# Optimization experiments

Measured on AMD Instinct MI355X. Metric: run time of the kernel, lower is better.

The kernel has to match this reference:

```python
import jax, jax.numpy as jnp
import numpy as np

LN_EPS = 1e-5
ROPE_BASE = 10000.0

def _rope2d_tables(height, width, dim):
    # dim = head_dim; split evenly between x (width) and y (height) axes
    dim_x = dim // 2
    dim_y = dim - dim_x
    inv_fx = 1.0 / (ROPE_BASE ** (jnp.arange(0, dim_x, 2, dtype=jnp.float32) / dim_x))
    inv_fy = 1.0 / (ROPE_BASE ** (jnp.arange(0, dim_y, 2, dtype=jnp.float32) / dim_y))
    fx = jnp.arange(width, dtype=jnp.float32)[:, None] * inv_fx[None, :]   # [W, dim_x/2]
    fy = jnp.arange(height, dtype=jnp.float32)[:, None] * inv_fy[None, :]  # [H, dim_y/2]
    cos_x = jnp.concatenate([jnp.cos(fx), jnp.cos(fx)], -1)  # [W, dim_x]
    sin_x = jnp.concatenate([jnp.sin(fx), jnp.sin(fx)], -1)
    cos_y = jnp.concatenate([jnp.cos(fy), jnp.cos(fy)], -1)  # [H, dim_y]
    sin_y = jnp.concatenate([jnp.sin(fy), jnp.sin(fy)], -1)
    cos2d = jnp.concatenate([jnp.broadcast_to(cos_x[None, :, :], (height, width, dim_x)),
                             jnp.broadcast_to(cos_y[:, None, :], (height, width, dim_y))], -1)
    sin2d = jnp.concatenate([jnp.broadcast_to(sin_x[None, :, :], (height, width, dim_x)),
                             jnp.broadcast_to(sin_y[:, None, :], (height, width, dim_y))], -1)
    return cos2d.reshape(height * width, dim), sin2d.reshape(height * width, dim)

def _apply_rope(x, cos, sin):
    # x: [..., S, D]; cos/sin broadcastable [S, D]
    d = x.shape[-1]
    x1, x2 = x[..., : d // 2], x[..., d // 2 :]
    rotated = jnp.concatenate([-x2, x1], -1)
    return x * cos + rotated * sin

def setup_inputs() -> dict:
    key = jax.random.key(0)
    ks = jax.random.split(key, 3)
    h = 1024
    x = jax.random.normal(ks[0], (1, 8192, h), dtype=jnp.float32)
    w_qkv = jax.random.normal(ks[1], (3 * h, h), dtype=jnp.float32) * (h ** -0.5)
    w_out = jax.random.normal(ks[2], (h, h), dtype=jnp.float32) * (h ** -0.5)
    return {
        "x": x, "w_qkv": w_qkv, "w_out": w_out,
        "ln_gamma": jnp.ones((h,), jnp.float32),
        "ln_beta": jnp.zeros((h,), jnp.float32),
        "height": 32, "width": 32, "frames": 8,
    }

def reference(x, w_qkv, w_out, ln_gamma, ln_beta, height, width, frames):
    B, S, hdim = x.shape
    num_heads = 16
    head_dim = hdim // num_heads
    spatial = height * width
    scale = head_dim ** -0.5

    # LayerNorm
    mu = jnp.mean(x, -1, keepdims=True)
    var = jnp.mean(jnp.square(x - mu), -1, keepdims=True)
    xn = (x - mu) * jax.lax.rsqrt(var + LN_EPS) * ln_gamma + ln_beta

    xn = xn.reshape(B * frames, spatial, hdim)
    qkv = (xn @ w_qkv.T).reshape(B * frames, spatial, 3, num_heads, head_dim)
    q, k, v = qkv[:, :, 0], qkv[:, :, 1], qkv[:, :, 2]  # [BF, S, H, D]
    q = jnp.transpose(q, (0, 2, 1, 3))  # [BF, H, S, D]
    k = jnp.transpose(k, (0, 2, 1, 3))
    v = jnp.transpose(v, (0, 2, 1, 3))

    cos, sin = _rope2d_tables(height, width, head_dim)  # [S, D]
    q = _apply_rope(q, cos, sin)
    k = _apply_rope(k, cos, sin)

    attn = jnp.einsum("bhqd,bhkd->bhqk", q, k) * scale
    attn = jax.nn.softmax(attn.astype(jnp.float32), axis=-1).astype(x.dtype)
    out = jnp.einsum("bhqk,bhkd->bhqd", attn, v)
    out = jnp.transpose(out, (0, 2, 1, 3)).reshape(B * frames, spatial, hdim)
    out = out @ w_out.T
    return out.reshape(B, S, hdim)
```

## Files before the change

### kernel.cpp

```cpp
#include <hip/hip_runtime.h>
#include <hip/hip_bf16.h>
#include <math.h>
#include <stdint.h>

typedef __bf16 bf16_t;
typedef bf16_t bf16x8 __attribute__((ext_vector_type(8)));
typedef bf16_t bf16x4 __attribute__((ext_vector_type(4)));
typedef float f32x4 __attribute__((ext_vector_type(4)));

#define GLOBAL_AS __attribute__((address_space(1)))
#define LDS_AS __attribute__((address_space(3)))

__device__ __forceinline__ void gload_lds16(const void* g, void* l) {
    __builtin_amdgcn_global_load_lds((const GLOBAL_AS unsigned int*)g,
                                     (LDS_AS unsigned int*)l, 16, 0, 0);
}

__device__ __forceinline__ f32x4 mfma16(bf16x8 a, bf16x8 b, f32x4 c) {
    return __builtin_amdgcn_mfma_f32_16x16x32_bf16(a, b, c, 0, 0, 0);
}

__global__ void prologue_kernel(const float* __restrict__ w_qkv, const float* __restrict__ w_out,
                                const float* __restrict__ x, const float* __restrict__ g,
                                const float* __restrict__ b,
                                bf16_t* __restrict__ wqb, bf16_t* __restrict__ wob,
                                bf16_t* __restrict__ xn,
                                float* __restrict__ cb, float* __restrict__ sb)
{
    __shared__ float red[8];
    const int bid = blockIdx.x;
    const int tid = threadIdx.x;

    if (bid < 3072) {
        const int i = bid * 256 + tid;
        const float4 v = ((const float4*)w_qkv)[i];
        bf16x4 o;
        o[0] = (bf16_t)v.x; o[1] = (bf16_t)v.y; o[2] = (bf16_t)v.z; o[3] = (bf16_t)v.w;
        *(bf16x4*)&wqb[(size_t)i * 4] = o;
    } else if (bid < 4096) {
        const int i = (bid - 3072) * 256 + tid;
        const float4 v = ((const float4*)w_out)[i];
        bf16x4 o;
        o[0] = (bf16_t)v.x; o[1] = (bf16_t)v.y; o[2] = (bf16_t)v.z; o[3] = (bf16_t)v.w;
        *(bf16x4*)&wob[(size_t)i * 4] = o;
    } else if (bid < 4352) {
        const int p = ((bid - 4096) << 2) | (tid >> 6);
        const int d = tid & 63;
        const int hh = p >> 5, ww = p & 31;
        const int idx = d & 15;
        const float invf = powf(10000.0f, -(float)idx / 16.0f);
        const float posv = (d >= 32) ? (float)hh : (float)ww;
        const float f = posv * invf;
        cb[p * 64 + d] = cosf(f);
        sb[p * 64 + d] = sinf(f);
    } else {
        const int row = bid - 4352;
        const float4 v = ((const float4*)(x + (size_t)row * 1024))[tid];
        float s  = v.x + v.y + v.z + v.w;
        float s2 = v.x * v.x + v.y * v.y + v.z * v.z + v.w * v.w;
        #pragma unroll
        for (int m = 1; m < 64; m <<= 1) {
            s  += __shfl_xor(s, m);
            s2 += __shfl_xor(s2, m);
        }
        const int wid = tid >> 6, lane = tid & 63;
        if (lane == 0) { red[wid] = s; red[4 + wid] = s2; }
        __syncthreads();
        s  = red[0] + red[1] + red[2] + red[3];
        s2 = red[4] + red[5] + red[6] + red[7];
        const float mu  = s * (1.0f / 1024.0f);
        const float var = s2 * (1.0f / 1024.0f) - mu * mu;
        const float rs  = rsqrtf(var + 1e-5f);
        const float4 gv = ((const float4*)g)[tid];
        const float4 bv = ((const float4*)b)[tid];
        bf16x4 o;
        o[0] = (bf16_t)((v.x - mu) * rs * gv.x + bv.x);
        o[1] = (bf16_t)((v.y - mu) * rs * gv.y + bv.y);
        o[2] = (bf16_t)((v.z - mu) * rs * gv.z + bv.z);
        o[3] = (bf16_t)((v.w - mu) * rs * gv.w + bv.w);
        *(bf16x4*)&xn[(size_t)row * 1024 + tid * 4] = o;
    }
}

template <int EPI>
__global__ __launch_bounds__(256, 2)
void gemm_bt(const bf16_t* __restrict__ A, const bf16_t* __restrict__ Bw,
             int M, int N,
             bf16_t* __restrict__ Qb, bf16_t* __restrict__ Kb, bf16_t* __restrict__ Vt,
             const float* __restrict__ cb, const float* __restrict__ sb,
             float* __restrict__ Cout)
{
    constexpr int K = 1024;
    __shared__ bf16_t Asm[2][128 * 64];
    __shared__ bf16_t Bsm[2][128 * 64];
    const int tid  = threadIdx.x;
    const int lane = tid & 63;
    const int wid  = tid >> 6;
    const int wr = wid >> 1, wc = wid & 1;
    const int lr = lane & 15;
    const int lg = lane >> 4;

    int lin = blockIdx.y * gridDim.x + blockIdx.x;
    const int cpx = (gridDim.x * gridDim.y) >> 3;
    lin = (lin & 7) * cpx + (lin >> 3);
    const int bx = lin % gridDim.x;
    const int by = lin / gridDim.x;
    const int bm = by * 128;
    const int bn = bx * 128;

    f32x4 acc[4][4] = {};

    const int r0 = tid >> 3;
    const int c8 = tid & 7;
    const int cx = c8 ^ (r0 & 7);

#define GSTAGE(b, k0) do { \
        _Pragma("unroll") \
        for (int i = 0; i < 4; ++i) { \
            gload_lds16(A  + (size_t)(bm + r0 + i * 32) * K + (k0) + cx * 8, (char*)&Asm[b][0] + i * 4096 + tid * 16); \
            gload_lds16(Bw + (size_t)(bn + r0 + i * 32) * K + (k0) + cx * 8, (char*)&Bsm[b][0] + i * 4096 + tid * 16); \
        } \
    } while (0)

    constexpr int nkt = K >> 6;
    GSTAGE(0, 0);
    GSTAGE(1, 64);

    #pragma unroll 2
    for (int t = 0; t < nkt; ++t) {
        const int cur = t & 1;
        if (t + 1 < nkt) asm volatile("s_waitcnt vmcnt(8)" ::: "memory");
        else             asm volatile("s_waitcnt vmcnt(0)" ::: "memory");
        __builtin_amdgcn_sched_barrier(0);
        __builtin_amdgcn_s_barrier();
        __builtin_amdgcn_sched_barrier(0);

        const bf16_t* As = &Asm[cur][0];
        const bf16_t* Bs = &Bsm[cur][0];
        bf16x8 af[2][4], bv[2][4];
        #pragma unroll
        for (int kk = 0; kk < 2; ++kk) {
            const int jx = ((kk * 4 + lg) ^ (lr & 7)) * 8;
            #pragma unroll
            for (int mi = 0; mi < 4; ++mi)
                af[kk][mi] = *(const bf16x8*)&As[(wr * 64 + mi * 16 + lr) * 64 + jx];
            #pragma unroll
            for (int nj = 0; nj < 4; ++nj)
                bv[kk][nj] = *(const bf16x8*)&Bs[(wc * 64 + nj * 16 + lr) * 64 + jx];
        }
        asm volatile("s_waitcnt lgkmcnt(0)" ::: "memory");
        __builtin_amdgcn_sched_barrier(0);
        __builtin_amdgcn_s_barrier();
        __builtin_amdgcn_sched_barrier(0);

        if (t + 2 < nkt) GSTAGE(cur, (t + 2) * 64);

        #pragma unroll
        for (int kk = 0; kk < 2; ++kk)
            #pragma unroll
            for (int mi = 0; mi < 4; ++mi)
                #pragma unroll
                for (int nj = 0; nj < 4; ++nj)
                    acc[mi][nj] = mfma16(af[kk][mi], bv[kk][nj], acc[mi][nj]);
    }
#undef GSTAGE

    if (EPI == 0) {
        const int sel = bn >> 10;
        if (sel < 2) {
            bf16_t* dst = sel ? Kb : Qb;
            const float qs = sel ? 1.0f : 0.18033688011112042f;
            #pragma unroll
            for (int mi = 0; mi < 4; ++mi) {
                #pragma unroll
                for (int nj = 0; nj < 2; ++nj) {
                    #pragma unroll
                    for (int r = 0; r < 4; ++r) {
                        const int m = bm + wr * 64 + mi * 16 + lg * 4 + r;
                        const int n_lo = bn + wc * 64 + nj * 16 + lr;
                        const int head = (n_lo >> 6) & 15;
                        const int d_lo = nj * 16 + lr;
                        const int pos  = m & 1023;
                        const int bfi  = m >> 10;
                        const float v_lo = acc[mi][nj][r];
                        const float v_hi = acc[mi][nj + 2][r];
                        const float c_lo = cb[pos * 64 + d_lo],      s_lo = sb[pos * 64 + d_lo];
                        const float c_hi = cb[pos * 64 + d_lo + 32], s_hi = sb[pos * 64 + d_lo + 32];
                        const size_t idx = (((size_t)(bfi * 16 + head)) << 16) + (size_t)pos * 64 + d_lo;
                        dst[idx]      = (bf16_t)((v_lo * c_lo - v_hi * s_lo) * qs);
                        dst[idx + 32] = (bf16_t)((v_hi * c_hi + v_lo * s_hi) * qs);
                    }
                }
            }
        } else {
            #pragma unroll
            for (int mi = 0; mi < 4; ++mi) {
                #pragma unroll
                for (int nj = 0; nj < 4; ++nj) {
                    bf16x4 pk;
                    #pragma unroll
                    for (int r = 0; r < 4; ++r) pk[r] = (bf16_t)acc[mi][nj][r];
                    const int m0 = bm + wr * 64 + mi * 16 + lg * 4;
                    const int n  = bn + wc * 64 + nj * 16 + lr;
                    const int head = (n >> 6) & 15;
                    const int d    = n & 63;
                    const int pos0 = m0 & 1023;
                    const int bfi  = m0 >> 10;
                    const int a = (pos0 >> 4) & 3, bb = (pos0 >> 2) & 3;
                    const int pos2 = (pos0 & ~63) | (32 * (a >> 1) + 8 * bb + 4 * (a & 1));
                    *(bf16x4*)&Vt[(((size_t)(bfi * 16 + head)) << 16) + (size_t)d * 1024 + pos2] = pk;
                }
            }
        }
    } else {
        #pragma unroll
        for (int mi = 0; mi < 4; ++mi)
            #pragma unroll
            for (int nj = 0; nj < 4; ++nj)
                #pragma unroll
                for (int r = 0; r < 4; ++r) {
                    const int m = bm + wr * 64 + mi * 16 + lg * 4 + r;
                    const int n = bn + wc * 64 + nj * 16 + lr;
                    Cout[(size_t)m * N + n] = acc[mi][nj][r];
                }
    }
}

__global__ __launch_bounds__(256, 4)
void attn_kernel(const bf16_t* __restrict__ Q, const bf16_t* __restrict__ Kg,
                 const bf16_t* __restrict__ Vt, bf16_t* __restrict__ AO)
{
    const int lin = blockIdx.x;
    const int bh  = (lin & 7) * 16 + ((lin >> 3) & 15);
    const int qt  = lin >> 7;
    const int tid = threadIdx.x;
    const int lane = tid & 63;
    const int wid  = tid >> 6;
    const int lr = lane & 15;
    const int lg = lane >> 4;

    __shared__ bf16_t Kbuf[2][64 * 64];
    __shared__ bf16_t Vbuf[2][64 * 64];

    const size_t hb = (size_t)bh << 16;
    const bf16_t* Qp = Q + hb;
    const char* Kc = (const char*)(Kg + hb);
    const char* Vc = (const char*)(Vt + hb);

    const int srow = tid >> 3;
    const int sch  = tid & 7;
    const int schx = sch ^ (srow & 7);
    const size_t gk0 = (size_t)srow * 128 + schx * 16;
    const size_t gk1 = (size_t)(srow + 32) * 128 + schx * 16;
    const size_t gv0 = (size_t)srow * 2048 + schx * 16;
    const size_t gv1 = (size_t)(srow + 32) * 2048 + schx * 16;

#define STAGE(b, t) do { \
        gload_lds16(Kc + (size_t)(t) * 8192 + gk0, (char*)&Kbuf[b][0] + tid * 16); \
        gload_lds16(Kc + (size_t)(t) * 8192 + gk1, (char*)&Kbuf[b][0] + 4096 + tid * 16); \
        gload_lds16(Vc + (size_t)(t) * 128  + gv0, (char*)&Vbuf[b][0] + tid * 16); \
        gload_lds16(Vc + (size_t)(t) * 128  + gv1, (char*)&Vbuf[b][0] + 4096 + tid * 16); \
    } while (0)

    bf16x8 qf[2][2];
    #pragma unroll
    for (int qtl = 0; qtl < 2; ++qtl)
        #pragma unroll
        for (int kk = 0; kk < 2; ++kk)
            qf[qtl][kk] = *(const bf16x8*)&Qp[(size_t)(qt * 128 + wid * 32 + qtl * 16 + lr) * 64 + kk * 32 + lg * 8];

    f32x4 o[2][4] = {};
    float lrow[2] = {};

    STAGE(0, 0);

    #pragma unroll 2
    for (int kt = 0; kt < 16; ++kt) {
        const int cur = kt & 1;
        __syncthreads();
        if (kt < 15) STAGE(cur ^ 1, kt + 1);

        const bf16_t* Kt_ = &Kbuf[cur][0];
        const bf16_t* Vt_ = &Vbuf[cur][0];

        f32x4 s[2][4] = {};
        __builtin_amdgcn_s_setprio(1);
        #pragma unroll
        for (int kk = 0; kk < 2; ++kk) {
            bf16x8 kf[4];
            #pragma unroll
            for (int k4 = 0; k4 < 4; ++k4)
                kf[k4] = *(const bf16x8*)&Kt_[(k4 * 16 + lr) * 64 + (((kk * 4 + lg) ^ (lr & 7)) * 8)];
            #pragma unroll
            for (int qtl = 0; qtl < 2; ++qtl)
                #pragma unroll
                for (int k4 = 0; k4 < 4; ++k4)
                    s[qtl][k4] = mfma16(kf[k4], qf[qtl][kk], s[qtl][k4]);
        }
        __builtin_amdgcn_s_setprio(0);

        #pragma unroll
        for (int qtl = 0; qtl < 2; ++qtl) {
            float ps = 0.0f;
            #pragma unroll
            for (int k4 = 0; k4 < 4; ++k4)
                #pragma unroll
                for (int r = 0; r < 4; ++r) {
                    const float p = exp2f(s[qtl][k4][r]);
                    s[qtl][k4][r] = p;
                    ps += p;
                }
            lrow[qtl] += ps;
        }

        bf16x8 pa[2][2];
        #pragma unroll
        for (int qtl = 0; qtl < 2; ++qtl)
            #pragma unroll
            for (int kk = 0; kk < 2; ++kk) {
                bf16x8 t;
                #pragma unroll
                for (int r = 0; r < 4; ++r) {
                    t[r]     = (bf16_t)s[qtl][2 * kk][r];
                    t[r + 4] = (bf16_t)s[qtl][2 * kk + 1][r];
                }
                pa[qtl][kk] = t;
            }

        __builtin_amdgcn_s_setprio(1);
        #pragma unroll
        for (int kk = 0; kk < 2; ++kk) {
            bf16x8 vf[4];
            #pragma unroll
            for (int dt = 0; dt < 4; ++dt)
                vf[dt] = *(const bf16x8*)&Vt_[(dt * 16 + lr) * 64 + (((kk * 4 + lg) ^ (lr & 7)) * 8)];
            #pragma unroll
            for (int qtl = 0; qtl < 2; ++qtl)
                #pragma unroll
                for (int dt = 0; dt < 4; ++dt)
                    o[qtl][dt] = mfma16(pa[qtl][kk], vf[dt], o[qtl][dt]);
        }
        __builtin_amdgcn_s_setprio(0);
    }
#undef STAGE

    #pragma unroll
    for (int qtl = 0; qtl < 2; ++qtl) {
        float l = lrow[qtl];
        l += __shfl_xor(l, 16);
        l += __shfl_xor(l, 32);
        lrow[qtl] = l;
    }

    const int bfi = bh >> 4;
    const int hh  = bh & 15;
    #pragma unroll
    for (int qtl = 0; qtl < 2; ++qtl) {
        #pragma unroll
        for (int r = 0; r < 4; ++r) {
            const float l = __shfl(lrow[qtl], (lane & 48) | (lg * 4 + r));
            const float inv = 1.0f / l;
            const int qrow = qt * 128 + wid * 32 + qtl * 16 + lg * 4 + r;
            const size_t mbase = (size_t)(bfi * 1024 + qrow) * 1024 + hh * 64;
            #pragma unroll
            for (int dt = 0; dt < 4; ++dt)
                AO[mbase + dt * 16 + lr] = (bf16_t)(o[qtl][dt][r] * inv);
        }
    }
}

extern "C" void kernel_launch(void* const* d_in, const int* in_sizes, int n_in,
                              void* d_out, int out_size, void* d_ws, size_t ws_size,
                              hipStream_t stream)
{
    const float* x     = (const float*)d_in[0];
    const float* w_qkv = (const float*)d_in[1];
    const float* w_out = (const float*)d_in[2];
    const float* ln_g  = (const float*)d_in[3];
    const float* ln_b  = (const float*)d_in[4];

    char* ws = (char*)d_ws;
    bf16_t* xn  = (bf16_t*)(ws);
    bf16_t* Qb  = (bf16_t*)(ws + ((size_t)16 << 20));
    bf16_t* Kb  = (bf16_t*)(ws + ((size_t)32 << 20));
    bf16_t* AO  = (bf16_t*)(ws + ((size_t)48 << 20));
    bf16_t* Vt  = (bf16_t*)(ws + ((size_t)64 << 20));
    bf16_t* wqb = (bf16_t*)(ws + ((size_t)80 << 20));
    bf16_t* wob = (bf16_t*)(ws + ((size_t)87 << 20));
    float*  cb  = (float*)(ws + ((size_t)90 << 20));
    float*  sb  = (float*)(ws + ((size_t)91 << 20));

    prologue_kernel<<<dim3(12544), dim3(256), 0, stream>>>(w_qkv, w_out, x, ln_g, ln_b,
                                                           wqb, wob, xn, cb, sb);
    gemm_bt<0><<<dim3(24, 64), dim3(256), 0, stream>>>(xn, wqb, 8192, 3072, Qb, Kb, Vt, cb, sb, nullptr);
    attn_kernel<<<dim3(1024), dim3(256), 0, stream>>>(Qb, Kb, Vt, AO);
    gemm_bt<1><<<dim3(8, 64), dim3(256), 0, stream>>>(AO, wob, 8192, 1024, nullptr, nullptr, nullptr, nullptr, nullptr, (float*)d_out);

    (void)in_sizes; (void)n_in; (void)out_size; (void)ws_size;
}
```

Baseline: 141.8 us.

## Load attention K/V fragments directly from global into registers, dropping LDS staging

The attention kernel no longer stages K and V tiles through double-buffered shared memory with barriers. Each wave now loads its MFMA fragments straight from global memory into registers, prefetching the next K tile while the current one is processed. Occupancy bounds drop from 4 to 2 blocks to make room for the extra registers. The GEMM inner MFMA loop is also wrapped in raised wave priority. This trades away LDS sharing across waves, so each wave fetches K/V itself, for fewer barriers and LDS traffic; it leans on L2/cache reuse and may lose latency hiding at lower occupancy.

```diff
diff --git a/kernel.cpp b/kernel.cpp
--- a/kernel.cpp
+++ b/kernel.cpp
@@ -155,6 +155,7 @@
 
         if (t + 2 < nkt) GSTAGE(cur, (t + 2) * 64);
 
+        __builtin_amdgcn_s_setprio(1);
         #pragma unroll
         for (int kk = 0; kk < 2; ++kk)
             #pragma unroll
@@ -162,6 +163,7 @@
                 #pragma unroll
                 for (int nj = 0; nj < 4; ++nj)
                     acc[mi][nj] = mfma16(af[kk][mi], bv[kk][nj], acc[mi][nj]);
+        __builtin_amdgcn_s_setprio(0);
     }
 #undef GSTAGE
 
@@ -226,7 +228,7 @@
     }
 }
 
-__global__ __launch_bounds__(256, 4)
+__global__ __launch_bounds__(256, 2)
 void attn_kernel(const bf16_t* __restrict__ Q, const bf16_t* __restrict__ Kg,
                  const bf16_t* __restrict__ Vt, bf16_t* __restrict__ AO)
 {
@@ -239,27 +241,57 @@
     const int lr = lane & 15;
     const int lg = lane >> 4;
 
-    __shared__ bf16_t Kbuf[2][64 * 64];
-    __shared__ bf16_t Vbuf[2][64 * 64];
-
     const size_t hb = (size_t)bh << 16;
     const bf16_t* Qp = Q + hb;
-    const char* Kc = (const char*)(Kg + hb);
-    const char* Vc = (const char*)(Vt + hb);
-
-    const int srow = tid >> 3;
-    const int sch  = tid & 7;
-    const int schx = sch ^ (srow & 7);
-    const size_t gk0 = (size_t)srow * 128 + schx * 16;
-    const size_t gk1 = (size_t)(srow + 32) * 128 + schx * 16;
-    const size_t gv0 = (size_t)srow * 2048 + schx * 16;
-    const size_t gv1 = (size_t)(srow + 32) * 2048 + schx * 16;
-
-#define STAGE(b, t) do { \
-        gload_lds16(Kc + (size_t)(t) * 8192 + gk0, (char*)&Kbuf[b][0] + tid * 16); \
-        gload_lds16(Kc + (size_t)(t) * 8192 + gk1, (char*)&Kbuf[b][0] + 4096 + tid * 16); \
-        gload_lds16(Vc + (size_t)(t) * 128  + gv0, (char*)&Vbuf[b][0] + tid * 16); \
-        gload_lds16(Vc + (size_t)(t) * 128  + gv1, (char*)&Vbuf[b][0] + 4096 + tid * 16); \
+    const bf16_t* Kp = Kg + hb + (size_t)lr * 64 + lg * 8;
+    const bf16_t* Vp = Vt + hb + (size_t)lr * 1024 + lg * 8;
+
+#define LOADK(dst, t) do { \
+        _Pragma("unroll") for (int kk = 0; kk < 2; ++kk) \
+        _Pragma("unroll") for (int k4 = 0; k4 < 4; ++k4) \
+            dst[kk][k4] = *(const bf16x8*)&Kp[(size_t)(t) * 4096 + k4 * 1024 + kk * 32]; \
+    } while (0)
+
+#define LOADV(dst, t) do { \
+        _Pragma("unroll") for (int kk = 0; kk < 2; ++kk) \
+        _Pragma("unroll") for (int dt = 0; dt < 4; ++dt) \
+            dst[kk][dt] = *(const bf16x8*)&Vp[dt * 16384 + (size_t)(t) * 64 + kk * 32]; \
+    } while (0)
+
+#define TILE_BODY(KF, VF) do { \
+        f32x4 s[2][4] = {}; \
+        __builtin_amdgcn_s_setprio(1); \
+        _Pragma("unroll") for (int kk = 0; kk < 2; ++kk) \
+        _Pragma("unroll") for (int qtl = 0; qtl < 2; ++qtl) \
+        _Pragma("unroll") for (int k4 = 0; k4 < 4; ++k4) \
+            s[qtl][k4] = mfma16(KF[kk][k4], qf[qtl][kk], s[qtl][k4]); \
+        __builtin_amdgcn_s_setprio(0); \
+        _Pragma("unroll") for (int qtl = 0; qtl < 2; ++qtl) { \
+            float ps = 0.0f; \
+            _Pragma("unroll") for (int k4 = 0; k4 < 4; ++k4) \
+            _Pragma("unroll") for (int r = 0; r < 4; ++r) { \
+                const float p = exp2f(s[qtl][k4][r]); \
+                s[qtl][k4][r] = p; \
+                ps += p; \
+            } \
+            lrow[qtl] += ps; \
+        } \
+        bf16x8 pa[2][2]; \
+        _Pragma("unroll") for (int qtl = 0; qtl < 2; ++qtl) \
+        _Pragma("unroll") for (int kk = 0; kk < 2; ++kk) { \
+            bf16x8 tpk; \
+            _Pragma("unroll") for (int r = 0; r < 4; ++r) { \
+                tpk[r]     = (bf16_t)s[qtl][2 * kk][r]; \
+                tpk[r + 4] = (bf16_t)s[qtl][2 * kk + 1][r]; \
+            } \
+            pa[qtl][kk] = tpk; \
+        } \
+        __builtin_amdgcn_s_setprio(1); \
+        _Pragma("unroll") for (int kk = 0; kk < 2; ++kk) \
+        _Pragma("unroll") for (int qtl = 0; qtl < 2; ++qtl) \
+        _Pragma("unroll") for (int dt = 0; dt < 4; ++dt) \
+            o[qtl][dt] = mfma16(pa[qtl][kk], VF[kk][dt], o[qtl][dt]); \
+        __builtin_amdgcn_s_setprio(0); \
     } while (0)
 
     bf16x8 qf[2][2];
@@ -272,77 +304,26 @@
     f32x4 o[2][4] = {};
     float lrow[2] = {};
 
-    STAGE(0, 0);
-
-    #pragma unroll 2
-    for (int kt = 0; kt < 16; ++kt) {
-        const int cur = kt & 1;
-        __syncthreads();
-        if (kt < 15) STAGE(cur ^ 1, kt + 1);
-
-        const bf16_t* Kt_ = &Kbuf[cur][0];
-        const bf16_t* Vt_ = &Vbuf[cur][0];
-
-        f32x4 s[2][4] = {};
-        __builtin_amdgcn_s_setprio(1);
-        #pragma unroll
-        for (int kk = 0; kk < 2; ++kk) {
-            bf16x8 kf[4];
-            #pragma unroll
-            for (int k4 = 0; k4 < 4; ++k4)
-                kf[k4] = *(const bf16x8*)&Kt_[(k4 * 16 + lr) * 64 + (((kk * 4 + lg) ^ (lr & 7)) * 8)];
-            #pragma unroll
-            for (int qtl = 0; qtl < 2; ++qtl)
-                #pragma unroll
-                for (int k4 = 0; k4 < 4; ++k4)
-                    s[qtl][k4] = mfma16(kf[k4], qf[qtl][kk], s[qtl][k4]);
-        }
-        __builtin_amdgcn_s_setprio(0);
-
-        #pragma unroll
-        for (int qtl = 0; qtl < 2; ++qtl) {
-            float ps = 0.0f;
-            #pragma unroll
-            for (int k4 = 0; k4 < 4; ++k4)
-                #pragma unroll
-                for (int r = 0; r < 4; ++r) {
-                    const float p = exp2f(s[qtl][k4][r]);
-                    s[qtl][k4][r] = p;
-                    ps += p;
-                }
-            lrow[qtl] += ps;
-        }
-
-        bf16x8 pa[2][2];
-        #pragma unroll
-        for (int qtl = 0; qtl < 2; ++qtl)
-            #pragma unroll
-            for (int kk = 0; kk < 2; ++kk) {
-                bf16x8 t;
-                #pragma unroll
-                for (int r = 0; r < 4; ++r) {
-                    t[r]     = (bf16_t)s[qtl][2 * kk][r];
-                    t[r + 4] = (bf16_t)s[qtl][2 * kk + 1][r];
-                }
-                pa[qtl][kk] = t;
-            }
-
-        __builtin_amdgcn_s_setprio(1);
-        #pragma unroll
-        for (int kk = 0; kk < 2; ++kk) {
-            bf16x8 vf[4];
-            #pragma unroll
-            for (int dt = 0; dt < 4; ++dt)
-                vf[dt] = *(const bf16x8*)&Vt_[(dt * 16 + lr) * 64 + (((kk * 4 + lg) ^ (lr & 7)) * 8)];
-            #pragma unroll
-            for (int qtl = 0; qtl < 2; ++qtl)
-                #pragma unroll
-                for (int dt = 0; dt < 4; ++dt)
-                    o[qtl][dt] = mfma16(pa[qtl][kk], vf[dt], o[qtl][dt]);
-        }
-        __builtin_amdgcn_s_setprio(0);
-    }
-#undef STAGE
+    bf16x8 kfA[2][4], kfB[2][4];
+    LOADK(kfA, 0);
+
+    for (int kt = 0; kt < 16; kt += 2) {
+        {
+            bf16x8 vf[2][4];
+            LOADV(vf, kt);
+            if (kt + 1 < 16) LOADK(kfB, kt + 1);
+            TILE_BODY(kfA, vf);
+        }
+        {
+            bf16x8 vf[2][4];
+            LOADV(vf, kt + 1);
+            if (kt + 2 < 16) LOADK(kfA, kt + 2);
+            TILE_BODY(kfB, vf);
+        }
+    }
+#undef LOADK
+#undef LOADV
+#undef TILE_BODY
 
     #pragma unroll
     for (int qtl = 0; qtl < 2; ++qtl) {
```

Result: slower. 206.6 us (+45.7%).
